# Kernel tuning notes

Measured on AMD Instinct MI355X. Metric: run time of the kernel, lower is better.

Reference implementation:

```python
import jax, jax.numpy as jnp
import numpy as np

D_MODEL = 1024
N_HEADS = 16
D_K = D_MODEL // N_HEADS
SCALE = 1.0 / np.sqrt(D_K).astype(np.float32)
NEG = -1000000000.0


def setup_inputs() -> dict:
    key = jax.random.key(0)
    ks = jax.random.split(key, 5)
    B, S = 2, 2048
    query = jax.random.normal(ks[0], (B, S, D_MODEL), dtype=jnp.float32)
    k_in = jax.random.normal(ks[1], (B, S, D_MODEL), dtype=jnp.float32)
    v_in = jax.random.normal(ks[2], (B, S, D_MODEL), dtype=jnp.float32)
    # causal mask, broadcast over batch and heads; 0 entries get -1e9
    mask = jnp.tril(jnp.ones((S, S), dtype=jnp.int32))[None, None, :, :]
    w_qkv = jax.random.normal(ks[3], (D_MODEL, 3 * D_MODEL), dtype=jnp.float32) * (1.0 / np.sqrt(D_MODEL))
    w_o = jax.random.normal(ks[4], (D_MODEL, D_MODEL), dtype=jnp.float32) * (1.0 / np.sqrt(D_MODEL))
    return {"query": query, "key": k_in, "value": v_in, "mask": mask, "w_qkv": w_qkv, "w_o": w_o}


def reference(query, key, value, mask, w_qkv, w_o):
    # NOTE: original module ignores `key`/`value`; q,k,v all come from `query`.
    B, S, _ = query.shape
    qkv = query @ w_qkv                       # [B,S,3D]
    q, k, v = jnp.split(qkv, 3, axis=-1)
    def heads(x):
        return x.reshape(B, S, N_HEADS, D_K).transpose(0, 2, 1, 3)  # [B,H,S,dk]
    Q, K, V = heads(q), heads(k), heads(v)
    scores = jnp.einsum('bhqd,bhkd->bhqk', Q, K) * SCALE            # [B,H,S,S]
    scores = jnp.where(mask == 0, NEG, scores)
    attn = jax.nn.softmax(scores, axis=-1)
    # Dropout(0.1) treated as eval-mode identity for a deterministic reference.
    context = jnp.einsum('bhqk,bhkd->bhqd', attn, V)                # [B,H,S,dk]
    context = context.transpose(0, 2, 1, 3).reshape(B, S, D_MODEL)
    return context @ w_o
```

## Files before the change

### kernel.cpp

```cpp
#include <hip/hip_runtime.h>
#include <stdint.h>


typedef __attribute__((ext_vector_type(8))) short bf16x8;
typedef __attribute__((ext_vector_type(4))) float f32x4;

#define LOG2E 1.44269504088896340736f
#define QSCALE (0.125f * LOG2E)

__device__ __forceinline__ unsigned short f2b(float f) {
  union { float f; unsigned int i; } x; x.f = f;
  unsigned int i = x.i;
  return (unsigned short)((i + 0x7FFFu + ((i >> 16) & 1u)) >> 16);
}

__device__ __forceinline__ void async16(const void* g, void* l) {
  __builtin_amdgcn_global_load_lds(
      (__attribute__((address_space(1))) void*)g,
      (__attribute__((address_space(3))) void*)l, 16, 0, 0);
}

__device__ __forceinline__ f32x4 mfma16(bf16x8 a, bf16x8 b, f32x4 c) {
  return __builtin_amdgcn_mfma_f32_16x16x32_bf16(a, b, c, 0, 0, 0);
}

__device__ __forceinline__ unsigned int fbits(float f) {
  union { float f; unsigned int i; } x; x.f = f;
  return x.i;
}

__global__ __launch_bounds__(256) void prep(
    const float* __restrict__ X, const float* __restrict__ Wqkv,
    const float* __restrict__ Wo, unsigned short* __restrict__ Xb,
    unsigned short* __restrict__ WqkvT, unsigned short* __restrict__ WoT) {
  __shared__ __align__(16) unsigned short Lt[64 * 64];
  const int bx = blockIdx.x;
  const int t = threadIdx.x;
  if (bx < 2048) {
    const size_t i = ((size_t)bx * 256 + t) * 8;
    float4 a = *(const float4*)(X + i);
    float4 b = *(const float4*)(X + i + 4);
    unsigned short e[8];
    e[0] = f2b(a.x); e[1] = f2b(a.y); e[2] = f2b(a.z); e[3] = f2b(a.w);
    e[4] = f2b(b.x); e[5] = f2b(b.y); e[6] = f2b(b.z); e[7] = f2b(b.w);
    *(uint4*)(Xb + i) = *(const uint4*)e;
    return;
  }
  const bool is_qkv = (bx < 2816);
  const int bid = is_qkv ? bx - 2048 : bx - 2816;
  const float* src = is_qkv ? Wqkv : Wo;
  unsigned short* dst = is_qkv ? WqkvT : WoT;
  const int Ccols = is_qkv ? 3072 : 1024;
  const int r0 = (bid & 15) * 64, c0 = (bid >> 4) * 64;
  const float s = (is_qkv && c0 < 1024) ? QSCALE : 1.0f;
#pragma unroll
  for (int it = 0; it < 4; ++it) {
    int c = it * 256 + t;
    int sr = c >> 4, co = (c & 15) * 4;
    float4 v = *(const float4*)(src + (size_t)(r0 + sr) * Ccols + c0 + co);
    Lt[(co + 0) * 64 + sr] = f2b(v.x * s);
    Lt[(co + 1) * 64 + sr] = f2b(v.y * s);
    Lt[(co + 2) * 64 + sr] = f2b(v.z * s);
    Lt[(co + 3) * 64 + sr] = f2b(v.w * s);
  }
  __syncthreads();
#pragma unroll
  for (int it = 0; it < 2; ++it) {
    int c = it * 256 + t;
    int dr = c >> 3, so = (c & 7) * 8;
    *(uint4*)(dst + (size_t)(c0 + dr) * 1024 + r0 + so) =
        *(const uint4*)(Lt + dr * 64 + so);
  }
}

__global__ __launch_bounds__(256) void gemm_qkv(
    const unsigned short* __restrict__ A, const unsigned short* __restrict__ Bt,
    unsigned short* __restrict__ C, unsigned short* __restrict__ Vt) {
  constexpr int K = 1024, N = 3072;
  __shared__ __align__(16) unsigned short Sm[16896];
  unsigned short* As = Sm;
  unsigned short* Bs = Sm + 8192;
  unsigned short* Lt = Sm;

  const int t = threadIdx.x;
  const int w = t >> 6, l = t & 63;
  const int m0 = blockIdx.y * 128, n0 = blockIdx.x * 128;
  const int wm = (w >> 1) * 64, wn = (w & 1) * 64;
  const int lrow = l & 15, lq = l >> 4;

  f32x4 acc[4][4] = {};

  for (int k0 = 0; k0 < K; k0 += 64) {
    __syncthreads();
#pragma unroll
    for (int r = 0; r < 4; ++r) {
      const int c = r * 256 + t;
      const int row = c >> 3;
      const int so = ((c & 7) ^ (row & 7)) * 8;
      async16(A + (size_t)(m0 + row) * K + k0 + so,
              As + (size_t)(r * 256 + t) * 8);
      async16(Bt + (size_t)(n0 + row) * K + k0 + so,
              Bs + (size_t)(r * 256 + t) * 8);
    }
    asm volatile("s_waitcnt vmcnt(0)" ::: "memory");
    __syncthreads();

#pragma unroll
    for (int kh = 0; kh < 2; ++kh) {
      bf16x8 af[4], bf[4];
      const int phys = ((kh * 4 + lq) ^ (lrow & 7)) * 8;
#pragma unroll
      for (int i = 0; i < 4; ++i)
        af[i] = *(const bf16x8*)(As + (wm + i * 16 + lrow) * 64 + phys);
#pragma unroll
      for (int j = 0; j < 4; ++j)
        bf[j] = *(const bf16x8*)(Bs + (wn + j * 16 + lrow) * 64 + phys);
#pragma unroll
      for (int i = 0; i < 4; ++i)
#pragma unroll
        for (int j = 0; j < 4; ++j)
          acc[i][j] = mfma16(af[i], bf[j], acc[i][j]);
    }
  }

  if (n0 < 2048) {
#pragma unroll
    for (int i = 0; i < 4; ++i)
#pragma unroll
      for (int j = 0; j < 4; ++j)
#pragma unroll
        for (int r = 0; r < 4; ++r) {
          int gr = m0 + wm + i * 16 + lq * 4 + r;
          int gc = n0 + wn + j * 16 + lrow;
          C[(size_t)gr * N + gc] = f2b(acc[i][j][r]);
        }
  } else {
    __syncthreads();
#pragma unroll
    for (int i = 0; i < 4; ++i)
#pragma unroll
      for (int j = 0; j < 4; ++j) {
        int col_loc = wn + j * 16 + lrow;
        int row_loc = wm + i * 16 + lq * 4;
        uint2 pk;
        pk.x = (unsigned int)f2b(acc[i][j][0]) |
               ((unsigned int)f2b(acc[i][j][1]) << 16);
        pk.y = (unsigned int)f2b(acc[i][j][2]) |
               ((unsigned int)f2b(acc[i][j][3]) << 16);
        *(uint2*)(Lt + col_loc * 132 + row_loc) = pk;
      }
    __syncthreads();
    const int b = m0 >> 11, s0 = m0 & 2047;
    const int vb0 = n0 - 2048;
#pragma unroll
    for (int rnd = 0; rnd < 8; ++rnd) {
      int vrow = rnd * 16 + (t >> 4);
      int sloc = (t & 15) * 8;
      int vcol = vb0 + vrow;
      int bh = b * 16 + (vcol >> 6);
      int d = vcol & 63;
      *(uint4*)(Vt + ((size_t)bh * 64 + d) * 2048 + s0 + sloc) =
          *(const uint4*)(Lt + vrow * 132 + sloc);
    }
  }
}

__global__ __launch_bounds__(256) void gemm_o(
    const unsigned short* __restrict__ A, const unsigned short* __restrict__ Bt,
    float* __restrict__ C, int M, int N, int K) {
  __shared__ __align__(16) unsigned short As[64 * 64];
  __shared__ __align__(16) unsigned short Bs[128 * 64];
  const int t = threadIdx.x;
  const int w = t >> 6, l = t & 63;
  const int m0 = blockIdx.y * 64, n0 = blockIdx.x * 128;
  const int wm = (w & 1) * 32, wn = (w >> 1) * 64;
  const int lrow = l & 15, lq = l >> 4;

  f32x4 acc[2][4] = {};

  for (int k0 = 0; k0 < K; k0 += 64) {
    __syncthreads();
#pragma unroll
    for (int r = 0; r < 2; ++r) {
      const int c = r * 256 + t;
      const int row = c >> 3;
      const int so = ((c & 7) ^ (row & 7)) * 8;
      async16(A + (size_t)(m0 + row) * K + k0 + so,
              As + (size_t)(r * 256 + t) * 8);
    }
#pragma unroll
    for (int r = 0; r < 4; ++r) {
      const int c = r * 256 + t;
      const int row = c >> 3;
      const int so = ((c & 7) ^ (row & 7)) * 8;
      async16(Bt + (size_t)(n0 + row) * K + k0 + so,
              Bs + (size_t)(r * 256 + t) * 8);
    }
    asm volatile("s_waitcnt vmcnt(0)" ::: "memory");
    __syncthreads();

#pragma unroll
    for (int kh = 0; kh < 2; ++kh) {
      bf16x8 af[2], bf[4];
      const int phys = ((kh * 4 + lq) ^ (lrow & 7)) * 8;
#pragma unroll
      for (int i = 0; i < 2; ++i)
        af[i] = *(const bf16x8*)(As + (wm + i * 16 + lrow) * 64 + phys);
#pragma unroll
      for (int j = 0; j < 4; ++j)
        bf[j] = *(const bf16x8*)(Bs + (wn + j * 16 + lrow) * 64 + phys);
#pragma unroll
      for (int i = 0; i < 2; ++i)
#pragma unroll
        for (int j = 0; j < 4; ++j)
          acc[i][j] = mfma16(af[i], bf[j], acc[i][j]);
    }
  }

#pragma unroll
  for (int i = 0; i < 2; ++i)
#pragma unroll
    for (int j = 0; j < 4; ++j)
#pragma unroll
      for (int r = 0; r < 4; ++r) {
        int gr = m0 + wm + i * 16 + lq * 4 + r;
        int gc = n0 + wn + j * 16 + lrow;
        C[(size_t)gr * N + gc] = acc[i][j][r];
      }
}

__global__ __launch_bounds__(512, 4) void attn_fwd(
    const unsigned short* __restrict__ qkv,
    const unsigned short* __restrict__ Vt,
    unsigned short* __restrict__ ctx) {
  __shared__ __align__(16) unsigned short Ks[2][64 * 64];
  __shared__ __align__(16) unsigned short Vs[2][64 * 64];
  __shared__ __align__(16) unsigned short Ps[8][16 * 72];

  const int idx = (blockIdx.x >> 3) + 2 * blockIdx.y;
  const int bh = (blockIdx.x & 7) * 4 + (idx >> 4);
  const int ti = idx & 15;
  const int b = bh >> 4, h = bh & 15;
  const int t = threadIdx.x;
  const int g = t >> 8;
  const int tl = t & 255;
  const int w = tl >> 6;
  const int gw = t >> 6;
  const int l = t & 63;
  const int lm = l & 15, lq = l >> 4;
  const int sw = lm & 7;
  const int c0 = (lq ^ sw) * 8;
  const int c1 = ((lq + 4) ^ sw) * 8;

  const int qt0[2] = {ti * 64, (31 - ti) * 64};
  const int ktmax = 31 - ti;
  const int nsup = (ktmax >> 1) + 1;

  const unsigned short* Qp = qkv + (size_t)(b * 2048) * 3072 + h * 64;
  const unsigned short* Kp = qkv + (size_t)(b * 2048) * 3072 + 1024 + h * 64;
  const unsigned short* Vb = Vt + (size_t)bh * 64 * 2048;

  bf16x8 qf[2][2];
#pragma unroll
  for (int qt = 0; qt < 2; ++qt) {
    const int qrow = qt0[qt] + w * 16 + lm;
    qf[qt][0] = *(const bf16x8*)(Qp + (size_t)qrow * 3072 + lq * 8);
    qf[qt][1] = *(const bf16x8*)(Qp + (size_t)qrow * 3072 + 32 + lq * 8);
  }

  f32x4 oacc[2][4] = {};
  float lsum[2] = {0.f, 0.f};

  for (int jj = 0; jj < nsup; ++jj) {
    const int kt = 2 * jj + g;
    const bool have = (kt <= ktmax);
    __syncthreads();
    if (have) {
      const int kk0 = kt * 64;
#pragma unroll
      for (int r = 0; r < 2; ++r) {
        int cl = r * 256 + tl;
        int row = cl >> 3, cp = cl & 7;
        int so = ((cp ^ (row & 7)) * 8);
        async16(Kp + (size_t)(kk0 + row) * 3072 + so,
                Ks[g] + (size_t)(r * 256 + w * 64) * 8);
        async16(Vb + (size_t)row * 2048 + kk0 + so,
                Vs[g] + (size_t)(r * 256 + w * 64) * 8);
      }
    }
    asm volatile("s_waitcnt vmcnt(0)" ::: "memory");
    __syncthreads();
    if (!have) continue;

    const unsigned short* Kc = Ks[g];
    const unsigned short* Vc = Vs[g];

    bf16x8 vf[8];
#pragma unroll
    for (int nt = 0; nt < 4; ++nt) {
      const unsigned short* vr = Vc + (nt * 16 + lm) * 64;
      vf[nt] = *(const bf16x8*)(vr + c0);
      vf[4 + nt] = *(const bf16x8*)(vr + c1);
    }

#pragma unroll
    for (int qt = 0; qt < 2; ++qt) {
      if (qt == 0 && kt > ti) continue;
      f32x4 sacc[4] = {};
      __builtin_amdgcn_s_setprio(1);
#pragma unroll
      for (int mt = 0; mt < 4; ++mt) {
        const unsigned short* kr = Kc + (mt * 16 + lm) * 64;
        bf16x8 bk0 = *(const bf16x8*)(kr + c0);
        bf16x8 bk1 = *(const bf16x8*)(kr + c1);
        sacc[mt] = mfma16(bk0, qf[qt][0], sacc[mt]);
        sacc[mt] = mfma16(bk1, qf[qt][1], sacc[mt]);
      }
      __builtin_amdgcn_s_setprio(0);

      const bool diag = (kt == ((qt == 0) ? ti : ktmax));
      const int qloc = w * 16 + lm;
#pragma unroll
      for (int mt = 0; mt < 4; ++mt) {
        float p0 = __builtin_amdgcn_exp2f(sacc[mt][0]);
        float p1 = __builtin_amdgcn_exp2f(sacc[mt][1]);
        float p2 = __builtin_amdgcn_exp2f(sacc[mt][2]);
        float p3 = __builtin_amdgcn_exp2f(sacc[mt][3]);
        if (diag) {
          const int kvb = mt * 16 + lq * 4;
          if (kvb + 0 > qloc) p0 = 0.f;
          if (kvb + 1 > qloc) p1 = 0.f;
          if (kvb + 2 > qloc) p2 = 0.f;
          if (kvb + 3 > qloc) p3 = 0.f;
        }
        lsum[qt] += (p0 + p1) + (p2 + p3);
        uint2 pk;
        pk.x = (fbits(p1) & 0xFFFF0000u) | (fbits(p0) >> 16);
        pk.y = (fbits(p3) & 0xFFFF0000u) | (fbits(p2) >> 16);
        *(uint2*)(&Ps[gw][lm * 72 + mt * 16 + lq * 4]) = pk;
      }
      asm volatile("s_waitcnt lgkmcnt(0)" ::: "memory");

      __builtin_amdgcn_s_setprio(1);
#pragma unroll
      for (int ks = 0; ks < 2; ++ks) {
        bf16x8 pa = *(const bf16x8*)(&Ps[gw][lm * 72 + ks * 32 + lq * 8]);
#pragma unroll
        for (int nt = 0; nt < 4; ++nt)
          oacc[qt][nt] = mfma16(pa, vf[ks * 4 + nt], oacc[qt][nt]);
      }
      __builtin_amdgcn_s_setprio(0);
    }
  }

#pragma unroll
  for (int qt = 0; qt < 2; ++qt) {
    lsum[qt] += __shfl_xor(lsum[qt], 16, 64);
    lsum[qt] += __shfl_xor(lsum[qt], 32, 64);
  }

  __syncthreads();
  float* fbuf[2] = {(float*)Ks, (float*)Vs};
  float* lbuf = (float*)Ps;
  if (g == 1) {
#pragma unroll
    for (int qt = 0; qt < 2; ++qt) {
#pragma unroll
      for (int nt = 0; nt < 4; ++nt)
#pragma unroll
        for (int r = 0; r < 4; ++r)
          fbuf[qt][(w * 16 + lq * 4 + r) * 64 + nt * 16 + lm] = oacc[qt][nt][r];
      if (l < 16) lbuf[qt * 64 + w * 16 + lm] = lsum[qt];
    }
  }
  __syncthreads();
  if (g == 0) {
#pragma unroll
    for (int qt = 0; qt < 2; ++qt) {
      const float ltot = lsum[qt] + lbuf[qt * 64 + w * 16 + lm];
      float rinv[4];
#pragma unroll
      for (int r = 0; r < 4; ++r)
        rinv[r] = 1.f / __shfl(ltot, lq * 4 + r, 64);
#pragma unroll
      for (int nt = 0; nt < 4; ++nt)
#pragma unroll
        for (int r = 0; r < 4; ++r) {
          float v = oacc[qt][nt][r] +
                    fbuf[qt][(w * 16 + lq * 4 + r) * 64 + nt * 16 + lm];
          size_t tok = (size_t)b * 2048 + qt0[qt] + w * 16 + lq * 4 + r;
          ctx[tok * 1024 + h * 64 + nt * 16 + lm] = f2b(v * rinv[r]);
        }
    }
  }
}

extern "C" void kernel_launch(void* const* d_in, const int* in_sizes, int n_in,
                              void* d_out, int out_size, void* d_ws,
                              size_t ws_size, hipStream_t stream) {
  const float* query = (const float*)d_in[0];
  const float* w_qkv = (const float*)d_in[4];
  const float* w_o = (const float*)d_in[5];
  float* out = (float*)d_out;

  unsigned short* ws = (unsigned short*)d_ws;
  unsigned short* wqkvT = ws;
  unsigned short* woT = wqkvT + (size_t)3072 * 1024;
  unsigned short* Xb = woT + (size_t)1024 * 1024;
  unsigned short* qkv = Xb + (size_t)4096 * 1024;
  unsigned short* Vt = qkv + (size_t)4096 * 3072;
  unsigned short* ctx = Xb;

  prep<<<dim3(3072), 256, 0, stream>>>(query, w_qkv, w_o, Xb, wqkvT, woT);
  gemm_qkv<<<dim3(24, 32), 256, 0, stream>>>(Xb, wqkvT, qkv, Vt);
  attn_fwd<<<dim3(16, 32), 512, 0, stream>>>(qkv, Vt, ctx);
  gemm_o<<<dim3(8, 64), 256, 0, stream>>>(ctx, woT, out, 4096, 1024, 1024);
}
```

Before: 199.6 us.

## Restructure causal attention into one query tile per block with double-buffered K/V prefetch

The attention kernel drops paired query tiles (ti and 31-ti) and the two-group split of the key sequence across 512 threads. Each 256-thread block now handles a single 64-row query tile, with blocks launched largest-tile-first. Inside the loop, the next K/V tile is prefetched asynchronously into the other buffer while the current one is computed, which removes the cross-group reduction at the end. The cost is load imbalance across blocks, now relying on launch order, plus V fragments being reloaded from LDS inside the PV loop.

```diff
diff --git a/kernel.cpp b/kernel.cpp
--- a/kernel.cpp
+++ b/kernel.cpp
@@ -229,170 +229,133 @@
       }
 }
 
-__global__ __launch_bounds__(512, 4) void attn_fwd(
+__global__ __launch_bounds__(256, 4) void attn_fwd(
     const unsigned short* __restrict__ qkv,
     const unsigned short* __restrict__ Vt,
     unsigned short* __restrict__ ctx) {
   __shared__ __align__(16) unsigned short Ks[2][64 * 64];
   __shared__ __align__(16) unsigned short Vs[2][64 * 64];
-  __shared__ __align__(16) unsigned short Ps[8][16 * 72];
-
-  const int idx = (blockIdx.x >> 3) + 2 * blockIdx.y;
-  const int bh = (blockIdx.x & 7) * 4 + (idx >> 4);
-  const int ti = idx & 15;
+  __shared__ __align__(16) unsigned short Ps[4][16 * 72];
+
+  const int bh = blockIdx.x;
+  const int ti = 31 - blockIdx.y;
   const int b = bh >> 4, h = bh & 15;
   const int t = threadIdx.x;
-  const int g = t >> 8;
-  const int tl = t & 255;
-  const int w = tl >> 6;
-  const int gw = t >> 6;
+  const int w = t >> 6;
   const int l = t & 63;
   const int lm = l & 15, lq = l >> 4;
   const int sw = lm & 7;
   const int c0 = (lq ^ sw) * 8;
   const int c1 = ((lq + 4) ^ sw) * 8;
 
-  const int qt0[2] = {ti * 64, (31 - ti) * 64};
-  const int ktmax = 31 - ti;
-  const int nsup = (ktmax >> 1) + 1;
-
   const unsigned short* Qp = qkv + (size_t)(b * 2048) * 3072 + h * 64;
   const unsigned short* Kp = qkv + (size_t)(b * 2048) * 3072 + 1024 + h * 64;
   const unsigned short* Vb = Vt + (size_t)bh * 64 * 2048;
 
-  bf16x8 qf[2][2];
-#pragma unroll
-  for (int qt = 0; qt < 2; ++qt) {
-    const int qrow = qt0[qt] + w * 16 + lm;
-    qf[qt][0] = *(const bf16x8*)(Qp + (size_t)qrow * 3072 + lq * 8);
-    qf[qt][1] = *(const bf16x8*)(Qp + (size_t)qrow * 3072 + 32 + lq * 8);
-  }
-
-  f32x4 oacc[2][4] = {};
-  float lsum[2] = {0.f, 0.f};
-
-  for (int jj = 0; jj < nsup; ++jj) {
-    const int kt = 2 * jj + g;
-    const bool have = (kt <= ktmax);
-    __syncthreads();
-    if (have) {
-      const int kk0 = kt * 64;
-#pragma unroll
-      for (int r = 0; r < 2; ++r) {
-        int cl = r * 256 + tl;
-        int row = cl >> 3, cp = cl & 7;
-        int so = ((cp ^ (row & 7)) * 8);
-        async16(Kp + (size_t)(kk0 + row) * 3072 + so,
-                Ks[g] + (size_t)(r * 256 + w * 64) * 8);
-        async16(Vb + (size_t)row * 2048 + kk0 + so,
-                Vs[g] + (size_t)(r * 256 + w * 64) * 8);
+  const int qrow = ti * 64 + w * 16 + lm;
+  bf16x8 qf0 = *(const bf16x8*)(Qp + (size_t)qrow * 3072 + lq * 8);
+  bf16x8 qf1 = *(const bf16x8*)(Qp + (size_t)qrow * 3072 + 32 + lq * 8);
+  asm volatile("s_waitcnt vmcnt(0)" ::: "memory");
+
+  const int srow0 = t >> 3, scp = t & 7;
+  const int srow1 = srow0 + 32;
+  const int sso0 = (scp ^ (srow0 & 7)) * 8;
+  const int sso1 = (scp ^ (srow1 & 7)) * 8;
+
+  f32x4 oacc[4] = {};
+  float lsum = 0.f;
+
+  {
+    async16(Kp + (size_t)srow0 * 3072 + sso0, Ks[0] + (size_t)t * 8);
+    async16(Vb + (size_t)srow0 * 2048 + sso0, Vs[0] + (size_t)t * 8);
+    async16(Kp + (size_t)srow1 * 3072 + sso1, Ks[0] + (size_t)(256 + t) * 8);
+    async16(Vb + (size_t)srow1 * 2048 + sso1, Vs[0] + (size_t)(256 + t) * 8);
+  }
+
+  for (int kt = 0; kt <= ti; ++kt) {
+    const int buf = kt & 1;
+    if (kt < ti) {
+      const int kk0 = (kt + 1) * 64;
+      async16(Kp + (size_t)(kk0 + srow0) * 3072 + sso0,
+              Ks[buf ^ 1] + (size_t)t * 8);
+      async16(Vb + (size_t)srow0 * 2048 + kk0 + sso0,
+              Vs[buf ^ 1] + (size_t)t * 8);
+      async16(Kp + (size_t)(kk0 + srow1) * 3072 + sso1,
+              Ks[buf ^ 1] + (size_t)(256 + t) * 8);
+      async16(Vb + (size_t)srow1 * 2048 + kk0 + sso1,
+              Vs[buf ^ 1] + (size_t)(256 + t) * 8);
+      asm volatile("s_waitcnt vmcnt(4)" ::: "memory");
+    } else {
+      asm volatile("s_waitcnt vmcnt(0)" ::: "memory");
+    }
+    __syncthreads();
+
+    const unsigned short* Kc = Ks[buf];
+    const unsigned short* Vc = Vs[buf];
+
+    f32x4 sacc[4] = {};
+    __builtin_amdgcn_s_setprio(1);
+#pragma unroll
+    for (int mt = 0; mt < 4; ++mt) {
+      const unsigned short* kr = Kc + (mt * 16 + lm) * 64;
+      bf16x8 bk0 = *(const bf16x8*)(kr + c0);
+      bf16x8 bk1 = *(const bf16x8*)(kr + c1);
+      sacc[mt] = mfma16(bk0, qf0, sacc[mt]);
+      sacc[mt] = mfma16(bk1, qf1, sacc[mt]);
+    }
+    __builtin_amdgcn_s_setprio(0);
+
+    const bool diag = (kt == ti);
+    const int qloc = w * 16 + lm;
+#pragma unroll
+    for (int mt = 0; mt < 4; ++mt) {
+      float p0 = __builtin_amdgcn_exp2f(sacc[mt][0]);
+      float p1 = __builtin_amdgcn_exp2f(sacc[mt][1]);
+      float p2 = __builtin_amdgcn_exp2f(sacc[mt][2]);
+      float p3 = __builtin_amdgcn_exp2f(sacc[mt][3]);
+      if (diag) {
+        const int kvb = mt * 16 + lq * 4;
+        if (kvb + 0 > qloc) p0 = 0.f;
+        if (kvb + 1 > qloc) p1 = 0.f;
+        if (kvb + 2 > qloc) p2 = 0.f;
+        if (kvb + 3 > qloc) p3 = 0.f;
       }
-    }
-    asm volatile("s_waitcnt vmcnt(0)" ::: "memory");
-    __syncthreads();
-    if (!have) continue;
-
-    const unsigned short* Kc = Ks[g];
-    const unsigned short* Vc = Vs[g];
-
-    bf16x8 vf[8];
-#pragma unroll
-    for (int nt = 0; nt < 4; ++nt) {
-      const unsigned short* vr = Vc + (nt * 16 + lm) * 64;
-      vf[nt] = *(const bf16x8*)(vr + c0);
-      vf[4 + nt] = *(const bf16x8*)(vr + c1);
-    }
-
-#pragma unroll
-    for (int qt = 0; qt < 2; ++qt) {
-      if (qt == 0 && kt > ti) continue;
-      f32x4 sacc[4] = {};
-      __builtin_amdgcn_s_setprio(1);
-#pragma unroll
-      for (int mt = 0; mt < 4; ++mt) {
-        const unsigned short* kr = Kc + (mt * 16 + lm) * 64;
-        bf16x8 bk0 = *(const bf16x8*)(kr + c0);
-        bf16x8 bk1 = *(const bf16x8*)(kr + c1);
-        sacc[mt] = mfma16(bk0, qf[qt][0], sacc[mt]);
-        sacc[mt] = mfma16(bk1, qf[qt][1], sacc[mt]);
+      lsum += (p0 + p1) + (p2 + p3);
+      uint2 pk;
+      pk.x = (fbits(p1) & 0xFFFF0000u) | (fbits(p0) >> 16);
+      pk.y = (fbits(p3) & 0xFFFF0000u) | (fbits(p2) >> 16);
+      *(uint2*)(&Ps[w][lm * 72 + mt * 16 + lq * 4]) = pk;
+    }
+    asm volatile("s_waitcnt lgkmcnt(0)" ::: "memory");
+
+    __builtin_amdgcn_s_setprio(1);
+#pragma unroll
+    for (int ks = 0; ks < 2; ++ks) {
+      bf16x8 pa = *(const bf16x8*)(&Ps[w][lm * 72 + ks * 32 + lq * 8]);
+#pragma unroll
+      for (int nt = 0; nt < 4; ++nt) {
+        const unsigned short* vr = Vc + (nt * 16 + lm) * 64;
+        bf16x8 vfr = *(const bf16x8*)(vr + (ks == 0 ? c0 : c1));
+        oacc[nt] = mfma16(pa, vfr, oacc[nt]);
       }
-      __builtin_amdgcn_s_setprio(0);
-
-      const bool diag = (kt == ((qt == 0) ? ti : ktmax));
-      const int qloc = w * 16 + lm;
-#pragma unroll
-      for (int mt = 0; mt < 4; ++mt) {
-        float p0 = __builtin_amdgcn_exp2f(sacc[mt][0]);
-        float p1 = __builtin_amdgcn_exp2f(sacc[mt][1]);
-        float p2 = __builtin_amdgcn_exp2f(sacc[mt][2]);
-        float p3 = __builtin_amdgcn_exp2f(sacc[mt][3]);
-        if (diag) {
-          const int kvb = mt * 16 + lq * 4;
-          if (kvb + 0 > qloc) p0 = 0.f;
-          if (kvb + 1 > qloc) p1 = 0.f;
-          if (kvb + 2 > qloc) p2 = 0.f;
-          if (kvb + 3 > qloc) p3 = 0.f;
-        }
-        lsum[qt] += (p0 + p1) + (p2 + p3);
-        uint2 pk;
-        pk.x = (fbits(p1) & 0xFFFF0000u) | (fbits(p0) >> 16);
-        pk.y = (fbits(p3) & 0xFFFF0000u) | (fbits(p2) >> 16);
-        *(uint2*)(&Ps[gw][lm * 72 + mt * 16 + lq * 4]) = pk;
-      }
-      asm volatile("s_waitcnt lgkmcnt(0)" ::: "memory");
-
-      __builtin_amdgcn_s_setprio(1);
-#pragma unroll
-      for (int ks = 0; ks < 2; ++ks) {
-        bf16x8 pa = *(const bf16x8*)(&Ps[gw][lm * 72 + ks * 32 + lq * 8]);
-#pragma unroll
-        for (int nt = 0; nt < 4; ++nt)
-          oacc[qt][nt] = mfma16(pa, vf[ks * 4 + nt], oacc[qt][nt]);
-      }
-      __builtin_amdgcn_s_setprio(0);
-    }
-  }
-
-#pragma unroll
-  for (int qt = 0; qt < 2; ++qt) {
-    lsum[qt] += __shfl_xor(lsum[qt], 16, 64);
-    lsum[qt] += __shfl_xor(lsum[qt], 32, 64);
-  }
-
-  __syncthreads();
-  float* fbuf[2] = {(float*)Ks, (float*)Vs};
-  float* lbuf = (float*)Ps;
-  if (g == 1) {
-#pragma unroll
-    for (int qt = 0; qt < 2; ++qt) {
-#pragma unroll
-      for (int nt = 0; nt < 4; ++nt)
-#pragma unroll
-        for (int r = 0; r < 4; ++r)
-          fbuf[qt][(w * 16 + lq * 4 + r) * 64 + nt * 16 + lm] = oacc[qt][nt][r];
-      if (l < 16) lbuf[qt * 64 + w * 16 + lm] = lsum[qt];
-    }
-  }
-  __syncthreads();
-  if (g == 0) {
-#pragma unroll
-    for (int qt = 0; qt < 2; ++qt) {
-      const float ltot = lsum[qt] + lbuf[qt * 64 + w * 16 + lm];
-      float rinv[4];
-#pragma unroll
-      for (int r = 0; r < 4; ++r)
-        rinv[r] = 1.f / __shfl(ltot, lq * 4 + r, 64);
-#pragma unroll
-      for (int nt = 0; nt < 4; ++nt)
-#pragma unroll
-        for (int r = 0; r < 4; ++r) {
-          float v = oacc[qt][nt][r] +
-                    fbuf[qt][(w * 16 + lq * 4 + r) * 64 + nt * 16 + lm];
-          size_t tok = (size_t)b * 2048 + qt0[qt] + w * 16 + lq * 4 + r;
-          ctx[tok * 1024 + h * 64 + nt * 16 + lm] = f2b(v * rinv[r]);
-        }
-    }
-  }
+    }
+    __builtin_amdgcn_s_setprio(0);
+
+    __syncthreads();
+  }
+
+  lsum += __shfl_xor(lsum, 16, 64);
+  lsum += __shfl_xor(lsum, 32, 64);
+  float rinv[4];
+#pragma unroll
+  for (int r = 0; r < 4; ++r) rinv[r] = 1.f / __shfl(lsum, lq * 4 + r, 64);
+#pragma unroll
+  for (int nt = 0; nt < 4; ++nt)
+#pragma unroll
+    for (int r = 0; r < 4; ++r) {
+      size_t tok = (size_t)b * 2048 + ti * 64 + w * 16 + lq * 4 + r;
+      ctx[tok * 1024 + h * 64 + nt * 16 + lm] = f2b(oacc[nt][r] * rinv[r]);
+    }
 }
 
 extern "C" void kernel_launch(void* const* d_in, const int* in_sizes, int n_in,
@@ -413,6 +376,6 @@
 
   prep<<<dim3(3072), 256, 0, stream>>>(query, w_qkv, w_o, Xb, wqkvT, woT);
   gemm_qkv<<<dim3(24, 32), 256, 0, stream>>>(Xb, wqkvT, qkv, Vt);
-  attn_fwd<<<dim3(16, 32), 512, 0, stream>>>(qkv, Vt, ctx);
+  attn_fwd<<<dim3(32, 32), 256, 0, stream>>>(qkv, Vt, ctx);
   gemm_o<<<dim3(8, 64), 256, 0, stream>>>(ctx, woT, out, 4096, 1024, 1024);
 }
```

Result: no change. 201.4 us (+0.9%).

## Replace paired causal query tiles with one tile per block, longest first

Applied to the files above, without the earlier changes.

The attention kernel previously gave each block two query tiles (ti and 31-ti) so the causal work was balanced, with both tiles sharing each loaded K/V tile. Now each block handles a single 64-row query tile, and the grid doubles to 1024 blocks ordered so the heaviest tiles (largest ti) launch first. The launch-bounds occupancy hint also rises from 4 to 6. This cuts register pressure and allows more concurrent blocks, but short tiles load their K/V without the reuse the paired scheme got, and load balance now depends on scheduling order.

```diff
diff --git a/kernel.cpp b/kernel.cpp
--- a/kernel.cpp
+++ b/kernel.cpp
@@ -229,7 +229,7 @@
       }
 }
 
-__global__ __launch_bounds__(512, 4) void attn_fwd(
+__global__ __launch_bounds__(512, 6) void attn_fwd(
     const unsigned short* __restrict__ qkv,
     const unsigned short* __restrict__ Vt,
     unsigned short* __restrict__ ctx) {
@@ -237,9 +237,8 @@
   __shared__ __align__(16) unsigned short Vs[2][64 * 64];
   __shared__ __align__(16) unsigned short Ps[8][16 * 72];
 
-  const int idx = (blockIdx.x >> 3) + 2 * blockIdx.y;
-  const int bh = (blockIdx.x & 7) * 4 + (idx >> 4);
-  const int ti = idx & 15;
+  const int bh = blockIdx.x;
+  const int ti = 31 - blockIdx.y;
   const int b = bh >> 4, h = bh & 15;
   const int t = threadIdx.x;
   const int g = t >> 8;
@@ -252,28 +251,22 @@
   const int c0 = (lq ^ sw) * 8;
   const int c1 = ((lq + 4) ^ sw) * 8;
 
-  const int qt0[2] = {ti * 64, (31 - ti) * 64};
-  const int ktmax = 31 - ti;
-  const int nsup = (ktmax >> 1) + 1;
-
   const unsigned short* Qp = qkv + (size_t)(b * 2048) * 3072 + h * 64;
   const unsigned short* Kp = qkv + (size_t)(b * 2048) * 3072 + 1024 + h * 64;
   const unsigned short* Vb = Vt + (size_t)bh * 64 * 2048;
 
-  bf16x8 qf[2][2];
-#pragma unroll
-  for (int qt = 0; qt < 2; ++qt) {
-    const int qrow = qt0[qt] + w * 16 + lm;
-    qf[qt][0] = *(const bf16x8*)(Qp + (size_t)qrow * 3072 + lq * 8);
-    qf[qt][1] = *(const bf16x8*)(Qp + (size_t)qrow * 3072 + 32 + lq * 8);
-  }
-
-  f32x4 oacc[2][4] = {};
-  float lsum[2] = {0.f, 0.f};
+  const int qrow = ti * 64 + w * 16 + lm;
+  bf16x8 qf0 = *(const bf16x8*)(Qp + (size_t)qrow * 3072 + lq * 8);
+  bf16x8 qf1 = *(const bf16x8*)(Qp + (size_t)qrow * 3072 + 32 + lq * 8);
+
+  f32x4 oacc[4] = {};
+  float lsum = 0.f;
+
+  const int nsup = (ti >> 1) + 1;
 
   for (int jj = 0; jj < nsup; ++jj) {
     const int kt = 2 * jj + g;
-    const bool have = (kt <= ktmax);
+    const bool have = (kt <= ti);
     __syncthreads();
     if (have) {
       const int kk0 = kt * 64;
@@ -303,95 +296,82 @@
       vf[4 + nt] = *(const bf16x8*)(vr + c1);
     }
 
-#pragma unroll
-    for (int qt = 0; qt < 2; ++qt) {
-      if (qt == 0 && kt > ti) continue;
-      f32x4 sacc[4] = {};
-      __builtin_amdgcn_s_setprio(1);
-#pragma unroll
-      for (int mt = 0; mt < 4; ++mt) {
-        const unsigned short* kr = Kc + (mt * 16 + lm) * 64;
-        bf16x8 bk0 = *(const bf16x8*)(kr + c0);
-        bf16x8 bk1 = *(const bf16x8*)(kr + c1);
-        sacc[mt] = mfma16(bk0, qf[qt][0], sacc[mt]);
-        sacc[mt] = mfma16(bk1, qf[qt][1], sacc[mt]);
-      }
-      __builtin_amdgcn_s_setprio(0);
-
-      const bool diag = (kt == ((qt == 0) ? ti : ktmax));
-      const int qloc = w * 16 + lm;
-#pragma unroll
-      for (int mt = 0; mt < 4; ++mt) {
-        float p0 = __builtin_amdgcn_exp2f(sacc[mt][0]);
-        float p1 = __builtin_amdgcn_exp2f(sacc[mt][1]);
-        float p2 = __builtin_amdgcn_exp2f(sacc[mt][2]);
-        float p3 = __builtin_amdgcn_exp2f(sacc[mt][3]);
-        if (diag) {
-          const int kvb = mt * 16 + lq * 4;
-          if (kvb + 0 > qloc) p0 = 0.f;
-          if (kvb + 1 > qloc) p1 = 0.f;
-          if (kvb + 2 > qloc) p2 = 0.f;
-          if (kvb + 3 > qloc) p3 = 0.f;
-        }
-        lsum[qt] += (p0 + p1) + (p2 + p3);
-        uint2 pk;
-        pk.x = (fbits(p1) & 0xFFFF0000u) | (fbits(p0) >> 16);
-        pk.y = (fbits(p3) & 0xFFFF0000u) | (fbits(p2) >> 16);
-        *(uint2*)(&Ps[gw][lm * 72 + mt * 16 + lq * 4]) = pk;
-      }
-      asm volatile("s_waitcnt lgkmcnt(0)" ::: "memory");
-
-      __builtin_amdgcn_s_setprio(1);
-#pragma unroll
-      for (int ks = 0; ks < 2; ++ks) {
-        bf16x8 pa = *(const bf16x8*)(&Ps[gw][lm * 72 + ks * 32 + lq * 8]);
-#pragma unroll
-        for (int nt = 0; nt < 4; ++nt)
-          oacc[qt][nt] = mfma16(pa, vf[ks * 4 + nt], oacc[qt][nt]);
-      }
-      __builtin_amdgcn_s_setprio(0);
-    }
-  }
-
-#pragma unroll
-  for (int qt = 0; qt < 2; ++qt) {
-    lsum[qt] += __shfl_xor(lsum[qt], 16, 64);
-    lsum[qt] += __shfl_xor(lsum[qt], 32, 64);
-  }
+    f32x4 sacc[4] = {};
+    __builtin_amdgcn_s_setprio(1);
+#pragma unroll
+    for (int mt = 0; mt < 4; ++mt) {
+      const unsigned short* kr = Kc + (mt * 16 + lm) * 64;
+      bf16x8 bk0 = *(const bf16x8*)(kr + c0);
+      bf16x8 bk1 = *(const bf16x8*)(kr + c1);
+      sacc[mt] = mfma16(bk0, qf0, sacc[mt]);
+      sacc[mt] = mfma16(bk1, qf1, sacc[mt]);
+    }
+    __builtin_amdgcn_s_setprio(0);
+
+    const bool diag = (kt == ti);
+    const int qloc = w * 16 + lm;
+#pragma unroll
+    for (int mt = 0; mt < 4; ++mt) {
+      float p0 = __builtin_amdgcn_exp2f(sacc[mt][0]);
+      float p1 = __builtin_amdgcn_exp2f(sacc[mt][1]);
+      float p2 = __builtin_amdgcn_exp2f(sacc[mt][2]);
+      float p3 = __builtin_amdgcn_exp2f(sacc[mt][3]);
+      if (diag) {
+        const int kvb = mt * 16 + lq * 4;
+        if (kvb + 0 > qloc) p0 = 0.f;
+        if (kvb + 1 > qloc) p1 = 0.f;
+        if (kvb + 2 > qloc) p2 = 0.f;
+        if (kvb + 3 > qloc) p3 = 0.f;
+      }
+      lsum += (p0 + p1) + (p2 + p3);
+      uint2 pk;
+      pk.x = (fbits(p1) & 0xFFFF0000u) | (fbits(p0) >> 16);
+      pk.y = (fbits(p3) & 0xFFFF0000u) | (fbits(p2) >> 16);
+      *(uint2*)(&Ps[gw][lm * 72 + mt * 16 + lq * 4]) = pk;
+    }
+    asm volatile("s_waitcnt lgkmcnt(0)" ::: "memory");
+
+    __builtin_amdgcn_s_setprio(1);
+#pragma unroll
+    for (int ks = 0; ks < 2; ++ks) {
+      bf16x8 pa = *(const bf16x8*)(&Ps[gw][lm * 72 + ks * 32 + lq * 8]);
+#pragma unroll
+      for (int nt = 0; nt < 4; ++nt)
+        oacc[nt] = mfma16(pa, vf[ks * 4 + nt], oacc[nt]);
+    }
+    __builtin_amdgcn_s_setprio(0);
+  }
+
+  lsum += __shfl_xor(lsum, 16, 64);
+  lsum += __shfl_xor(lsum, 32, 64);
 
   __syncthreads();
-  float* fbuf[2] = {(float*)Ks, (float*)Vs};
+  float* fbuf = (float*)Ks;
   float* lbuf = (float*)Ps;
   if (g == 1) {
 #pragma unroll
-    for (int qt = 0; qt < 2; ++qt) {
-#pragma unroll
-      for (int nt = 0; nt < 4; ++nt)
-#pragma unroll
-        for (int r = 0; r < 4; ++r)
-          fbuf[qt][(w * 16 + lq * 4 + r) * 64 + nt * 16 + lm] = oacc[qt][nt][r];
-      if (l < 16) lbuf[qt * 64 + w * 16 + lm] = lsum[qt];
-    }
+    for (int nt = 0; nt < 4; ++nt)
+#pragma unroll
+      for (int r = 0; r < 4; ++r)
+        fbuf[(w * 16 + lq * 4 + r) * 64 + nt * 16 + lm] = oacc[nt][r];
+    if (l < 16) lbuf[w * 16 + lm] = lsum;
   }
   __syncthreads();
   if (g == 0) {
-#pragma unroll
-    for (int qt = 0; qt < 2; ++qt) {
-      const float ltot = lsum[qt] + lbuf[qt * 64 + w * 16 + lm];
-      float rinv[4];
-#pragma unroll
-      for (int r = 0; r < 4; ++r)
-        rinv[r] = 1.f / __shfl(ltot, lq * 4 + r, 64);
-#pragma unroll
-      for (int nt = 0; nt < 4; ++nt)
-#pragma unroll
-        for (int r = 0; r < 4; ++r) {
-          float v = oacc[qt][nt][r] +
-                    fbuf[qt][(w * 16 + lq * 4 + r) * 64 + nt * 16 + lm];
-          size_t tok = (size_t)b * 2048 + qt0[qt] + w * 16 + lq * 4 + r;
-          ctx[tok * 1024 + h * 64 + nt * 16 + lm] = f2b(v * rinv[r]);
-        }
-    }
+    const float ltot = lsum + lbuf[w * 16 + lm];
+    float rinv[4];
+#pragma unroll
+    for (int r = 0; r < 4; ++r)
+      rinv[r] = 1.f / __shfl(ltot, lq * 4 + r, 64);
+#pragma unroll
+    for (int nt = 0; nt < 4; ++nt)
+#pragma unroll
+      for (int r = 0; r < 4; ++r) {
+        float v = oacc[nt][r] +
+                  fbuf[(w * 16 + lq * 4 + r) * 64 + nt * 16 + lm];
+        size_t tok = (size_t)b * 2048 + ti * 64 + w * 16 + lq * 4 + r;
+        ctx[tok * 1024 + h * 64 + nt * 16 + lm] = f2b(v * rinv[r]);
+      }
   }
 }
 
@@ -413,6 +393,6 @@
 
   prep<<<dim3(3072), 256, 0, stream>>>(query, w_qkv, w_o, Xb, wqkvT, woT);
   gemm_qkv<<<dim3(24, 32), 256, 0, stream>>>(Xb, wqkvT, qkv, Vt);
-  attn_fwd<<<dim3(16, 32), 512, 0, stream>>>(qkv, Vt, ctx);
+  attn_fwd<<<dim3(32, 32), 512, 0, stream>>>(qkv, Vt, ctx);
   gemm_o<<<dim3(8, 64), 256, 0, stream>>>(ctx, woT, out, 4096, 1024, 1024);
 }
```

New measurement: 268.0 us. 1.34x slower.
